# Kernel optimization log

Hardware: AMD Instinct MI355X
Metric: run time of the kernel (lower is better)

## Reference

```python
import jax, jax.numpy as jnp
import numpy as np

NL, H, PD, NH, NB = 4, 256, 64, 4, 65
B, L, AA = 2, 384, 48
DH = H // NH
MAX_REL = 32


def _ln(x, g, b):
    m = x.mean(-1, keepdims=True)
    v = ((x - m) ** 2).mean(-1, keepdims=True)
    return (x - m) * jax.lax.rsqrt(v + 1e-5) * g + b


def setup_inputs() -> dict:
    key = jax.random.key(0)
    ks = iter(jax.random.split(key, 64))
    w = lambda *s: jax.random.normal(next(ks), s, jnp.float32) * 0.02
    return dict(
        x=jax.random.normal(next(ks), (B, L, AA), jnp.float32),
        rp_w=w(AA, H), rp_b=jnp.zeros((H,), jnp.float32),
        pos_embed=w(L, H),
        pii_w=w(H, PD), pii_b=jnp.zeros((PD,), jnp.float32),
        pij_w=w(H, PD), pij_b=jnp.zeros((PD,), jnp.float32),
        rel_emb=w(2 * MAX_REL + 2, PD),
        ln_seq_g=jnp.ones((NL, H), jnp.float32), ln_seq_b=jnp.zeros((NL, H), jnp.float32),
        ln_pair_g=jnp.ones((NL, PD), jnp.float32), ln_pair_b=jnp.zeros((NL, PD), jnp.float32),
        pb_w=w(NL, PD, NH),
        in_w=w(NL, H, 3 * H), in_b=jnp.zeros((NL, 3 * H), jnp.float32),
        out_w=w(NL, H, H), out_b=jnp.zeros((NL, H), jnp.float32),
        ff_ln_g=jnp.ones((NL, H), jnp.float32), ff_ln_b=jnp.zeros((NL, H), jnp.float32),
        ff_w1=w(NL, H, 4 * H), ff_b1=jnp.zeros((NL, 4 * H), jnp.float32),
        ff_w2=w(NL, 4 * H, H), ff_b2=jnp.zeros((NL, H), jnp.float32),
        pu_ln_g=jnp.ones((NL, PD), jnp.float32), pu_ln_b=jnp.zeros((NL, PD), jnp.float32),
        pu_w1=w(NL, PD, PD), pu_b1=jnp.zeros((NL, PD), jnp.float32),
        pu_w2=w(NL, PD, PD), pu_b2=jnp.zeros((NL, PD), jnp.float32),
        outer_w=w(NL, 2 * H, PD), outer_b=jnp.zeros((NL, PD), jnp.float32),
        dh_ln_g=jnp.ones((PD,), jnp.float32), dh_ln_b=jnp.zeros((PD,), jnp.float32),
        dh_w1=w(PD, PD), dh_b1=jnp.zeros((PD,), jnp.float32),
        dh_w2=w(PD, NB), dh_b2=jnp.zeros((NB,), jnp.float32),
    )


def reference(x, rp_w, rp_b, pos_embed, pii_w, pii_b, pij_w, pij_b, rel_emb,
              ln_seq_g, ln_seq_b, ln_pair_g, ln_pair_b, pb_w, in_w, in_b,
              out_w, out_b, ff_ln_g, ff_ln_b, ff_w1, ff_b1, ff_w2, ff_b2,
              pu_ln_g, pu_ln_b, pu_w1, pu_b1, pu_w2, pu_b2, outer_w, outer_b,
              dh_ln_g, dh_ln_b, dh_w1, dh_b1, dh_w2, dh_b2):
    Bx, Lx, _ = x.shape
    gelu = lambda t: jax.nn.gelu(t, approximate=False)  # torch nn.GELU default (erf)
    h = x @ rp_w + rp_b + pos_embed[:Lx][None]
    # pair init: outer sum of two linear projections + clipped rel-pos embedding
    pair = (h @ pii_w + pii_b)[:, :, None, :] + (h @ pij_w + pij_b)[:, None, :, :]
    idx = jnp.arange(Lx)
    rel = jnp.clip(idx[None, :] - idx[:, None], -MAX_REL, MAX_REL) + MAX_REL  # (L,L)
    pair = pair + rel_emb[rel][None]
    for i in range(NL):
        seq_n = _ln(h, ln_seq_g[i], ln_seq_b[i])
        bias = _ln(pair, ln_pair_g[i], ln_pair_b[i]) @ pb_w[i]  # (B,L,L,NH)
        mask = bias.mean(axis=(0, 3))  # torch: permute->reshape(B*NH,L,L)->mean(0)
        qkv = seq_n @ in_w[i] + in_b[i]
        q, k, v = jnp.split(qkv, 3, axis=-1)
        q = q.reshape(Bx, Lx, NH, DH)
        k = k.reshape(Bx, Lx, NH, DH)
        v = v.reshape(Bx, Lx, NH, DH)
        scores = jnp.einsum('blhd,bmhd->bhlm', q, k) / float(np.sqrt(DH)) + mask
        attn = jax.nn.softmax(scores, axis=-1)
        o = jnp.einsum('bhlm,bmhd->blhd', attn, v).reshape(Bx, Lx, H)
        h = h + o @ out_w[i] + out_b[i]
        h = h + gelu(_ln(h, ff_ln_g[i], ff_ln_b[i]) @ ff_w1[i] + ff_b1[i]) @ ff_w2[i] + ff_b2[i]
        # outer_proj(cat([h_i, h_j])) == h@W[:H] outer-summed with h@W[H:]
        oi = h @ outer_w[i][:H]
        oj = h @ outer_w[i][H:]
        outer = oi[:, :, None, :] + oj[:, None, :, :] + outer_b[i]  # (B,L,L,PD)
        pair = pair + gelu(_ln(outer, pu_ln_g[i], pu_ln_b[i]) @ pu_w1[i] + pu_b1[i]) @ pu_w2[i] + pu_b2[i]
    logits = gelu(_ln(pair, dh_ln_g, dh_ln_b) @ dh_w1 + dh_b1) @ dh_w2 + dh_b2
    return (logits + jnp.swapaxes(logits, 1, 2)) / 2.0
```

## Files before the change

kernel.cpp:

```cpp
#include <hip/hip_runtime.h>
#include <math.h>

#define LSEQ 384
#define HD 256
#define PDIM 64
#define NHEAD 4
#define NBINS 65
#define BATCH 2
#define NTT (LSEQ / 16)
#define NTRI (NTT * (NTT + 1) / 2)

typedef __attribute__((ext_vector_type(8))) short bf16x8;
typedef __attribute__((ext_vector_type(16))) float f32x16;
typedef __attribute__((ext_vector_type(4))) float f32x4;
typedef __attribute__((ext_vector_type(4))) unsigned u32x4;
typedef __attribute__((ext_vector_type(4))) short s16x4;
#define MFMA32(a, b, c) __builtin_amdgcn_mfma_f32_32x32x16_bf16(a, b, c, 0, 0, 0)

template<int CTRL, int RMASK>
__device__ __forceinline__ float dpp_sum_step(float v) {
    int x = __builtin_amdgcn_update_dpp(0, __float_as_int(v), CTRL, RMASK, 0xf, true);
    return v + __int_as_float(x);
}
template<int CTRL, int RMASK>
__device__ __forceinline__ float dpp_max_step(float v) {
    int x = __builtin_amdgcn_update_dpp(__float_as_int(v), __float_as_int(v), CTRL, RMASK, 0xf, false);
    return fmaxf(v, __int_as_float(x));
}
__device__ __forceinline__ float wsum(float v) {
    v = dpp_sum_step<0x111, 0xf>(v);
    v = dpp_sum_step<0x112, 0xf>(v);
    v = dpp_sum_step<0x114, 0xf>(v);
    v = dpp_sum_step<0x118, 0xf>(v);
    v = dpp_sum_step<0x142, 0xa>(v);
    v = dpp_sum_step<0x143, 0xc>(v);
    return __int_as_float(__builtin_amdgcn_readlane(__float_as_int(v), 63));
}
__device__ __forceinline__ float wmax(float v) {
    v = dpp_max_step<0x111, 0xf>(v);
    v = dpp_max_step<0x112, 0xf>(v);
    v = dpp_max_step<0x114, 0xf>(v);
    v = dpp_max_step<0x118, 0xf>(v);
    v = dpp_max_step<0x142, 0xa>(v);
    v = dpp_max_step<0x143, 0xc>(v);
    return __int_as_float(__builtin_amdgcn_readlane(__float_as_int(v), 63));
}
__device__ __forceinline__ float gelu_erf(float x) {
    return 0.5f * x * (1.0f + erff(x * 0.70710678f));
}

__device__ __forceinline__ unsigned short f2bf(float x) {
    unsigned u = __float_as_uint(x);
    unsigned r = (u + 0x7fff + ((u >> 16) & 1)) >> 16;
    return (unsigned short)r;
}
__device__ __forceinline__ float bf2f(unsigned short h) {
    return __uint_as_float(((unsigned)h) << 16);
}
__device__ __forceinline__ void split_bf(float x, unsigned short& h, unsigned short& l) {
    h = f2bf(x);
    l = f2bf(x - bf2f(h));
}

__device__ __forceinline__ unsigned cvt_pk_bf(float lo, float hi) {
    unsigned r;
    asm("v_cvt_pk_bf16_f32 %0, %1, %2" : "=v"(r) : "v"(lo), "v"(hi));
    return r;
}
__device__ __forceinline__ void pack8(const float* v, u32x4& h, u32x4& l) {
#pragma unroll
    for (int j = 0; j < 4; ++j) {
        float a = v[2 * j], b = v[2 * j + 1];
        unsigned hp = cvt_pk_bf(a, b);
        float ra = a - __uint_as_float(hp << 16);
        float rb = b - __uint_as_float(hp & 0xffff0000u);
        h[j] = hp;
        l[j] = cvt_pk_bf(ra, rb);
    }
}
__device__ __forceinline__ bf16x8 as_bf(u32x4 x) {
    union { u32x4 u; bf16x8 b; } c; c.u = x; return c.b;
}
__device__ __forceinline__ bf16x8 ld8(const short* p) {
    s16x4 a = *(const s16x4*)p;
    s16x4 b = *(const s16x4*)(p + 4);
    bf16x8 r;
    r[0] = a[0]; r[1] = a[1]; r[2] = a[2]; r[3] = a[3];
    r[4] = b[0]; r[5] = b[1]; r[6] = b[2]; r[7] = b[3];
    return r;
}

__global__ void k_h_init(const float* __restrict__ x, const float* __restrict__ rp_w,
                         const float* __restrict__ rp_b, const float* __restrict__ pos,
                         float* __restrict__ h) {
    __shared__ float xs[48];
    int row = blockIdx.x;
    int l = row % LSEQ;
    int t = threadIdx.x;
    if (t < 48) xs[t] = x[row * 48 + t];
    __syncthreads();
    float acc = rp_b[t] + pos[l * HD + t];
#pragma unroll 8
    for (int a = 0; a < 48; ++a) acc += xs[a] * rp_w[a * HD + t];
    h[row * HD + t] = acc;
}

__global__ void k_proj2(const float* __restrict__ h, const float* __restrict__ wA,
                        const float* __restrict__ wB, const float* __restrict__ bA,
                        const float* __restrict__ bB, int center,
                        float* __restrict__ pA, float* __restrict__ pB) {
    __shared__ float hs[HD];
    int row = blockIdx.x;
    int t = threadIdx.x;
    hs[t] = h[row * HD + t];
    hs[t + 128] = h[row * HD + t + 128];
    __syncthreads();
    int col = t & 63;
    const float* w = (t < 64) ? wA : wB;
    const float* bias = (t < 64) ? bA : bB;
    float acc = bias ? bias[col] : 0.0f;
#pragma unroll 8
    for (int a = 0; a < HD; ++a) acc += hs[a] * w[a * PDIM + col];
    if (center) {
        float mean = wsum(acc) * (1.0f / PDIM);
        acc -= mean;
    }
    float* p = (t < 64) ? pA : pB;
    p[row * PDIM + col] = acc;
}

__global__ void __launch_bounds__(64) k_pair_init2(
    const float* __restrict__ pi, const float* __restrict__ pj,
    const float* __restrict__ rel_emb, const float* __restrict__ gpb,
    const float* __restrict__ cbv, float* __restrict__ pair,
    float* __restrict__ mask_out) {
    __shared__ __align__(16) float pt[32][65];
    int blk = blockIdx.x;
    int row = blk / 12, seg = blk % 12;
    int b = row / LSEQ, i = row % LSEQ;
    int t = threadIdx.x;
    int pl = t & 31, hq = t >> 5;
    int j0 = seg * 32;
    float piv = pi[row * 64 + t];
    const float* pjb = pj + ((size_t)b * LSEQ + j0) * 64;
#pragma unroll 8
    for (int j = 0; j < 32; ++j) {
        int r = j0 + j - i; r = r < -32 ? -32 : (r > 32 ? 32 : r); r += 32;
        pt[j][t] = piv + pjb[j * 64 + t] + rel_emb[r * 64 + t];
    }
    __syncthreads();
    float4* dst4 = (float4*)(pair + ((size_t)row * LSEQ + j0) * 64);
    for (int n = t; n < 512; n += 64) {
        int r2 = n >> 4, c4 = (n & 15) << 2;
        float4 g4 = { pt[r2][c4], pt[r2][c4 + 1], pt[r2][c4 + 2], pt[r2][c4 + 3] };
        dst4[n] = g4;
    }
    float vv[32];
    float sv = 0.0f;
#pragma unroll
    for (int c = 0; c < 32; ++c) { vv[c] = pt[pl][hq * 32 + c]; sv += vv[c]; }
    sv += __shfl_xor(sv, 32);
    float mean = sv * (1.0f / PDIM);
    float sd2 = 0.0f, sdg = 0.0f;
#pragma unroll
    for (int c = 0; c < 32; ++c) {
        float d = vv[c] - mean;
        sd2 = fmaf(d, d, sd2);
        sdg = fmaf(d, gpb[hq * 32 + c], sdg);
    }
    sd2 += __shfl_xor(sd2, 32);
    sdg += __shfl_xor(sdg, 32);
    float rsv = rsqrtf(sd2 * (1.0f / PDIM) + 1e-5f);
    float dot = rsv * sdg + cbv[0];
    if (hq == 0)
        atomicAdd(mask_out + i * LSEQ + j0 + pl, dot * (1.0f / (BATCH * NHEAD)));
}

__global__ void k_prep(const float* __restrict__ pu_ln_g, const float* __restrict__ pu_ln_b,
                       const float* __restrict__ pu_w1, const float* __restrict__ pu_b1,
                       const float* __restrict__ pu_w2,
                       const float* __restrict__ dh_ln_g, const float* __restrict__ dh_ln_b,
                       const float* __restrict__ dh_w1, const float* __restrict__ dh_b1,
                       const float* __restrict__ dh_w2,
                       unsigned short* __restrict__ w1hT, unsigned short* __restrict__ w1lT,
                       unsigned short* __restrict__ w2hT, unsigned short* __restrict__ w2lT,
                       float* __restrict__ b1p, float* __restrict__ w2c) {
    int i = blockIdx.x;
    int c = threadIdx.x;
    const float *g, *bb, *w1, *b1, *w2;
    int w2s;
    if (i < 4) { g = pu_ln_g + i * 64; bb = pu_ln_b + i * 64; w1 = pu_w1 + i * 4096;
                 b1 = pu_b1 + i * 64; w2 = pu_w2 + i * 4096; w2s = 64; }
    else       { g = dh_ln_g; bb = dh_ln_b; w1 = dh_w1; b1 = dh_b1; w2 = dh_w2; w2s = 65; }
    float accb = b1[c];
    for (int k = 0; k < 64; ++k) {
        float wv = w1[k * 64 + c];
        accb += bb[k] * wv;
        unsigned short h, l;
        split_bf(g[k] * wv, h, l);
        w1hT[i * 4096 + c * 64 + k] = h;
        w1lT[i * 4096 + c * 64 + k] = l;
        split_bf(w2[k * w2s + c], h, l);
        w2hT[i * 4096 + c * 64 + k] = h;
        w2lT[i * 4096 + c * 64 + k] = l;
    }
    b1p[i * 64 + c] = accb;
    if (i == 4) w2c[c] = dh_w2[c * 65 + 64];
}

__global__ void k_maskprep(const float* __restrict__ g, const float* __restrict__ bb,
                           const float* __restrict__ pbw, float* __restrict__ gp,
                           float* __restrict__ cb) {
    int li = blockIdx.x;
    int c = threadIdx.x;
    const float* pw = pbw + li * PDIM * NHEAD;
    float pbs = pw[c * 4] + pw[c * 4 + 1] + pw[c * 4 + 2] + pw[c * 4 + 3];
    gp[li * 64 + c] = g[li * 64 + c] * pbs;
    float s = wsum(bb[li * 64 + c] * pbs);
    if (c == 0) cb[li] = s;
}

__global__ void k_split_T(const float* __restrict__ src, unsigned short* __restrict__ dh,
                          unsigned short* __restrict__ dl, int K, int N,
                          int tiles_k, int tiles_n, size_t sstride, size_t dstride) {
    __shared__ float lds[64][65];
    int bid = blockIdx.x;
    int tpl = tiles_k * tiles_n;
    int layer = bid / tpl;
    int rest = bid % tpl;
    int kt = rest / tiles_n, nt = rest % tiles_n;
    const float* s = src + layer * sstride;
    int t = threadIdx.x, c = t & 63, r0 = t >> 6;
    for (int r = r0; r < 64; r += 4)
        lds[r][c] = s[(size_t)(kt * 64 + r) * N + nt * 64 + c];
    __syncthreads();
    unsigned short* oh = dh + layer * dstride;
    unsigned short* ol = dl + layer * dstride;
    for (int r = r0; r < 64; r += 4) {
        float v = lds[c][r];
        unsigned short h, l;
        split_bf(v, h, l);
        size_t o = (size_t)(nt * 64 + r) * K + kt * 64 + c;
        oh[o] = h;
        ol[o] = l;
    }
}

template<bool GELU>
__global__ void __launch_bounds__(64) k_gemm(
    const float* __restrict__ X, const unsigned short* __restrict__ wTh,
    const unsigned short* __restrict__ wTl, const float* __restrict__ bias,
    const float* __restrict__ R, float* __restrict__ OUT, int K, int N) {
    int idx = blockIdx.x;
    int lane = threadIdx.x & 63;
    int pl = lane & 31, hq = lane >> 5;
    int ntiles = N >> 5;
    int mt = idx / ntiles, nt = idx % ntiles;
    const float* xr = X + (size_t)(mt * 32 + pl) * K + 8 * hq;
    const unsigned short* bh = wTh + (size_t)(nt * 32 + pl) * K + 8 * hq;
    const unsigned short* bl = wTl + (size_t)(nt * 32 + pl) * K + 8 * hq;
    int n = nt * 32 + pl;
    float bv = bias[n];
    f32x16 acc;
#pragma unroll
    for (int r = 0; r < 16; ++r) {
        int mr = mt * 32 + (r & 3) + 8 * (r >> 2) + 4 * hq;
        acc[r] = bv + (R ? R[(size_t)mr * N + n] : 0.0f);
    }
#pragma unroll 4
    for (int s = 0; s < K; s += 16) {
        const f32x4* x4 = (const f32x4*)(xr + s);
        f32x4 xa = x4[0], xb = x4[1];
        float xv[8];
#pragma unroll
        for (int j = 0; j < 4; ++j) { xv[j] = xa[j]; xv[4 + j] = xb[j]; }
        u32x4 ah, al;
        pack8(xv, ah, al);
        bf16x8 bhv = *(const bf16x8*)(bh + s);
        bf16x8 blv = *(const bf16x8*)(bl + s);
        acc = MFMA32(as_bf(ah), bhv, acc);
        acc = MFMA32(as_bf(al), bhv, acc);
        acc = MFMA32(as_bf(ah), blv, acc);
    }
#pragma unroll
    for (int r = 0; r < 16; ++r) {
        int mr = mt * 32 + (r & 3) + 8 * (r >> 2) + 4 * hq;
        float v = acc[r];
        OUT[(size_t)mr * N + n] = GELU ? gelu_erf(v) : v;
    }
}

__global__ void k_ln_seq(const float* __restrict__ h, const float* __restrict__ g,
                         const float* __restrict__ b, float* __restrict__ out) {
    __shared__ float red[8];
    int row = blockIdx.x;
    int t = threadIdx.x;
    int w = t >> 6, lane = t & 63;
    float v = h[row * HD + t];
    float s = wsum(v);
    if (lane == 0) red[w] = s;
    __syncthreads();
    float mean = (red[0] + red[1] + red[2] + red[3]) * (1.0f / HD);
    float d = v - mean;
    float q = wsum(d * d);
    if (lane == 0) red[4 + w] = q;
    __syncthreads();
    float var = (red[4] + red[5] + red[6] + red[7]) * (1.0f / HD);
    out[row * HD + t] = d * rsqrtf(var + 1e-5f) * g[t] + b[t];
}

__global__ void k_attn(const float* __restrict__ qkv, const float* __restrict__ mask,
                       float* __restrict__ o) {
    __shared__ __align__(16) float qs[64];
    __shared__ float sc[LSEQ];
    __shared__ float red[8];
    __shared__ float op[4][64];
    int bid = blockIdx.x;
    int l = bid % LSEQ;
    int nh = (bid / LSEQ) & 3;
    int b = bid / (LSEQ * NHEAD);
    int t = threadIdx.x;
    int w = t >> 6, lane = t & 63;
    const float* qbase = qkv + ((size_t)(b * LSEQ + l)) * 768 + nh * 64;
    if (t < 64) qs[t] = qbase[t];
    __syncthreads();
    float lmax = -1e30f;
    float myv[2];
#pragma unroll
    for (int it = 0; it < 2; ++it) {
        int m = t + it * 256;
        if (m < LSEQ) {
            const float* kb = qkv + ((size_t)(b * LSEQ + m)) * 768 + 256 + nh * 64;
            const float4* k4 = (const float4*)kb;
            const float4* q4 = (const float4*)qs;
            float acc = 0.0f;
#pragma unroll
            for (int a = 0; a < 16; ++a) {
                float4 kv = k4[a], qv = q4[a];
                acc += qv.x * kv.x + qv.y * kv.y + qv.z * kv.z + qv.w * kv.w;
            }
            float s = acc * 0.125f + mask[l * LSEQ + m];
            myv[it] = s;
            lmax = fmaxf(lmax, s);
        } else myv[it] = -1e30f;
    }
    float wm = wmax(lmax);
    if (lane == 0) red[w] = wm;
    __syncthreads();
    float gmax = fmaxf(fmaxf(red[0], red[1]), fmaxf(red[2], red[3]));
    float lsum = 0.0f;
#pragma unroll
    for (int it = 0; it < 2; ++it) {
        int m = t + it * 256;
        if (m < LSEQ) {
            float e = expf(myv[it] - gmax);
            sc[m] = e;
            lsum += e;
        }
    }
    float ws = wsum(lsum);
    if (lane == 0) red[4 + w] = ws;
    __syncthreads();
    float inv = 1.0f / (red[4] + red[5] + red[6] + red[7]);
    int d = t & 63, gq = t >> 6;
    float part = 0.0f;
    for (int m = gq * 96; m < (gq + 1) * 96; ++m)
        part += sc[m] * qkv[((size_t)(b * LSEQ + m)) * 768 + 512 + nh * 64 + d];
    op[gq][d] = part;
    __syncthreads();
    if (t < 64) {
        float ov = (op[0][t] + op[1][t] + op[2][t] + op[3][t]) * inv;
        o[((size_t)(b * LSEQ + l)) * HD + nh * 64 + t] = ov;
    }
}

template<bool DIST>
__global__ void __launch_bounds__(256) k_pair_upd(
    const float* __restrict__ ojc,
    const float* __restrict__ oic,
    const unsigned short* __restrict__ w1hT, const unsigned short* __restrict__ w1lT,
    const float* __restrict__ b1p,
    const unsigned short* __restrict__ w2hT, const unsigned short* __restrict__ w2lT,
    const float* __restrict__ b2, float* __restrict__ pair,
    const float* __restrict__ gpb, const float* __restrict__ cbv,
    float* __restrict__ mask_out,
    const unsigned short* __restrict__ dw1h, const unsigned short* __restrict__ dw1l,
    const float* __restrict__ db1p,
    const unsigned short* __restrict__ dw2h, const unsigned short* __restrict__ dw2l,
    const float* __restrict__ w2c, const float* __restrict__ db2,
    float* __restrict__ outg) {
    __shared__ __align__(16) char smem[DIST ? 33344 : 17472];
    short (*lw)[64][68] = (short (*)[64][68])smem;
    int blk = blockIdx.x;
    int row = blk / 3, seg = blk % 3;
    int b = row / LSEQ;
    int t = threadIdx.x;
    int wave = t >> 6, lane = t & 63;
    int pl = lane & 31, hq = lane >> 5;
    int jj = wave * 32 + pl;
    int p = seg * 128 + jj;
    const float* ojr = ojc + ((size_t)b * LSEQ + p) * 64;
    const float* oir = oic + (size_t)row * 64;
    float* prp = pair + ((size_t)row * LSEQ + p) * 64;

#define STAGE2(srcA, srcB) \
    for (int idx = t; idx < 2048; idx += 256) { \
        int rr2 = idx >> 5, cc2 = (idx & 31) * 2; \
        *(unsigned*)&lw[0][rr2][cc2] = *(const unsigned*)(srcA + rr2 * 64 + cc2); \
        *(unsigned*)&lw[1][rr2][cc2] = *(const unsigned*)(srcB + rr2 * 64 + cc2); \
    }

    float v[32];
    {
        const f32x4* a4 = (const f32x4*)ojr;
        const f32x4* c4 = (const f32x4*)oir;
#pragma unroll
        for (int s = 0; s < 4; ++s) {
            f32x4 a = a4[4 * s + 2 * hq], aa = a4[4 * s + 2 * hq + 1];
            f32x4 c = c4[4 * s + 2 * hq], cc = c4[4 * s + 2 * hq + 1];
#pragma unroll
            for (int j = 0; j < 4; ++j) {
                v[8 * s + j] = a[j] + c[j];
                v[8 * s + 4 + j] = aa[j] + cc[j];
            }
        }
    }
    STAGE2(w1hT, w1lT)

    float ss = 0.0f;
#pragma unroll
    for (int i = 0; i < 32; ++i) ss = fmaf(v[i], v[i], ss);
    ss += __shfl_xor(ss, 32);
    float rs = rsqrtf(ss * (1.0f / PDIM) + 1e-5f);
#pragma unroll
    for (int i = 0; i < 32; ++i) v[i] *= rs;
    u32x4 zh[4], zl[4];
#pragma unroll
    for (int s = 0; s < 4; ++s) pack8(v + 8 * s, zh[s], zl[s]);

    const f32x4* b14 = (const f32x4*)b1p;
    f32x4 bi0[4], bi1[4];
#pragma unroll
    for (int g = 0; g < 4; ++g) { bi0[g] = b14[2 * g + hq]; bi1[g] = b14[8 + 2 * g + hq]; }

    __syncthreads();

    f32x16 acc0, acc1;
#pragma unroll
    for (int r = 0; r < 16; ++r) {
        acc0[r] = bi0[r >> 2][r & 3];
        acc1[r] = bi1[r >> 2][r & 3];
    }
#pragma unroll
    for (int s = 0; s < 4; ++s) {
        int ko = 16 * s + 8 * hq;
        bf16x8 a0h = ld8(&lw[0][pl][ko]);
        bf16x8 a0l = ld8(&lw[1][pl][ko]);
        bf16x8 a1h = ld8(&lw[0][32 + pl][ko]);
        bf16x8 a1l = ld8(&lw[1][32 + pl][ko]);
        bf16x8 zhs = as_bf(zh[s]), zls = as_bf(zl[s]);
        acc0 = MFMA32(a0h, zhs, acc0);
        acc0 = MFMA32(a0h, zls, acc0);
        acc0 = MFMA32(a0l, zhs, acc0);
        acc1 = MFMA32(a1h, zhs, acc1);
        acc1 = MFMA32(a1h, zls, acc1);
        acc1 = MFMA32(a1l, zhs, acc1);
    }
    __syncthreads();
    STAGE2(w2hT, w2lT)

    float u0[16], u1[16];
#pragma unroll
    for (int r = 0; r < 16; ++r) { u0[r] = gelu_erf(acc0[r]); u1[r] = gelu_erf(acc1[r]); }

    f32x4 r0[4], r1[4], q0[4], q1[4];
    {
        const f32x4* pr4 = (const f32x4*)prp;
        const f32x4* b24 = (const f32x4*)b2;
#pragma unroll
        for (int g = 0; g < 4; ++g) {
            r0[g] = pr4[2 * g + hq];
            r1[g] = pr4[8 + 2 * g + hq];
            q0[g] = b24[2 * g + hq];
            q1[g] = b24[8 + 2 * g + hq];
        }
    }

    float rA0[4], rB0[4], rA1[4], rB1[4];
#pragma unroll
    for (int i = 0; i < 4; ++i) {
        rA0[i] = __shfl_xor(hq ? u0[i] : u0[4 + i], 32);
        rB0[i] = __shfl_xor(hq ? u0[8 + i] : u0[12 + i], 32);
        rA1[i] = __shfl_xor(hq ? u1[i] : u1[4 + i], 32);
        rB1[i] = __shfl_xor(hq ? u1[8 + i] : u1[12 + i], 32);
    }
    u32x4 uh[4], ul[4];
#pragma unroll
    for (int s = 0; s < 4; ++s) {
        int tt = s >> 1, q = s & 1;
        float fg[8];
#pragma unroll
        for (int i = 0; i < 4; ++i) {
            float own_f = q ? (tt ? u1[8 + i] : u0[8 + i]) : (tt ? u1[i] : u0[i]);
            float own_s = q ? (tt ? u1[12 + i] : u0[12 + i]) : (tt ? u1[4 + i] : u0[4 + i]);
            float rcv   = q ? (tt ? rB1[i] : rB0[i]) : (tt ? rA1[i] : rA0[i]);
            fg[i]     = hq ? rcv : own_f;
            fg[4 + i] = hq ? own_s : rcv;
        }
        pack8(fg, uh[s], ul[s]);
    }

    __syncthreads();

    f32x16 c0, c1;
#pragma unroll
    for (int r = 0; r < 16; ++r) {
        int g = r >> 2, i = r & 3;
        c0[r] = q0[g][i] + r0[g][i];
        c1[r] = q1[g][i] + r1[g][i];
    }
#pragma unroll
    for (int s = 0; s < 4; ++s) {
        int ko = 16 * s + 8 * hq;
        bf16x8 a0h = ld8(&lw[0][pl][ko]);
        bf16x8 a0l = ld8(&lw[1][pl][ko]);
        bf16x8 a1h = ld8(&lw[0][32 + pl][ko]);
        bf16x8 a1l = ld8(&lw[1][32 + pl][ko]);
        bf16x8 uhs = as_bf(uh[s]), uls = as_bf(ul[s]);
        c0 = MFMA32(a0h, uhs, c0);
        c0 = MFMA32(a0h, uls, c0);
        c0 = MFMA32(a0l, uhs, c0);
        c1 = MFMA32(a1h, uhs, c1);
        c1 = MFMA32(a1h, uls, c1);
        c1 = MFMA32(a1l, uhs, c1);
    }

    if constexpr (!DIST) {
        const f32x4* gp4 = (const f32x4*)gpb;
        f32x4 gp0[4], gp1[4];
#pragma unroll
        for (int g = 0; g < 4; ++g) { gp0[g] = gp4[2 * g + hq]; gp1[g] = gp4[8 + 2 * g + hq]; }
        float sv = 0.0f;
#pragma unroll
        for (int r = 0; r < 16; ++r) sv += c0[r] + c1[r];
        sv += __shfl_xor(sv, 32);
        float mean = sv * (1.0f / PDIM);
        float sd2 = 0.0f, sdg = 0.0f;
#pragma unroll 4
        for (int r = 0; r < 16; ++r) {
            int g = r >> 2, i = r & 3;
            float d0 = c0[r] - mean, d1 = c1[r] - mean;
            sd2 = fmaf(d0, d0, sd2);
            sd2 = fmaf(d1, d1, sd2);
            sdg = fmaf(d0, gp0[g][i], sdg);
            sdg = fmaf(d1, gp1[g][i], sdg);
        }
        sd2 += __shfl_xor(sd2, 32);
        sdg += __shfl_xor(sdg, 32);
        float rsv = rsqrtf(sd2 * (1.0f / PDIM) + 1e-5f);
        float dot = rsv * sdg + cbv[0];
        if (hq == 0)
            atomicAdd(mask_out + (row % LSEQ) * LSEQ + p, dot * (1.0f / (BATCH * NHEAD)));
        f32x4* pw4 = (f32x4*)prp;
#pragma unroll
        for (int g = 0; g < 4; ++g) {
            f32x4 s0, s1;
#pragma unroll
            for (int i = 0; i < 4; ++i) { s0[i] = c0[4 * g + i]; s1[i] = c1[4 * g + i]; }
            pw4[2 * g + hq] = s0;
            pw4[8 + 2 * g + hq] = s1;
        }
    } else {
        float ra[4], rb[4], rc[4], rd[4];
#pragma unroll
        for (int i = 0; i < 4; ++i) {
            ra[i] = __shfl_xor(hq ? c0[i] : c0[4 + i], 32);
            rb[i] = __shfl_xor(hq ? c0[8 + i] : c0[12 + i], 32);
            rc[i] = __shfl_xor(hq ? c1[i] : c1[4 + i], 32);
            rd[i] = __shfl_xor(hq ? c1[8 + i] : c1[12 + i], 32);
        }
        float v2[32];
#pragma unroll
        for (int i = 0; i < 4; ++i) {
            v2[i]      = hq ? ra[i] : c0[i];
            v2[4 + i]  = hq ? c0[4 + i] : ra[i];
            v2[8 + i]  = hq ? rb[i] : c0[8 + i];
            v2[12 + i] = hq ? c0[12 + i] : rb[i];
            v2[16 + i] = hq ? rc[i] : c1[i];
            v2[20 + i] = hq ? c1[4 + i] : rc[i];
            v2[24 + i] = hq ? rd[i] : c1[8 + i];
            v2[28 + i] = hq ? c1[12 + i] : rd[i];
        }
        __syncthreads();
        STAGE2(dw1h, dw1l)

        float sm = 0.0f;
#pragma unroll
        for (int i = 0; i < 32; ++i) sm += v2[i];
        sm += __shfl_xor(sm, 32);
        float mean = sm * (1.0f / PDIM);
        float ss2 = 0.0f;
#pragma unroll
        for (int i = 0; i < 32; ++i) { v2[i] -= mean; ss2 = fmaf(v2[i], v2[i], ss2); }
        ss2 += __shfl_xor(ss2, 32);
        float rs2 = rsqrtf(ss2 * (1.0f / PDIM) + 1e-5f);
#pragma unroll
        for (int i = 0; i < 32; ++i) v2[i] *= rs2;
#pragma unroll
        for (int s = 0; s < 4; ++s) pack8(v2 + 8 * s, zh[s], zl[s]);

        const f32x4* d14 = (const f32x4*)db1p;
        const f32x4* d24 = (const f32x4*)db2;
        const f32x4* wc4 = (const f32x4*)w2c;
        f32x4 di0[4], di1[4], e0[4], e1[4], wc0[4], wc1[4];
#pragma unroll
        for (int g = 0; g < 4; ++g) {
            di0[g] = d14[2 * g + hq]; di1[g] = d14[8 + 2 * g + hq];
            e0[g] = d24[2 * g + hq];  e1[g] = d24[8 + 2 * g + hq];
            wc0[g] = wc4[2 * g + hq]; wc1[g] = wc4[8 + 2 * g + hq];
        }
        __syncthreads();

#pragma unroll
        for (int r = 0; r < 16; ++r) {
            acc0[r] = di0[r >> 2][r & 3];
            acc1[r] = di1[r >> 2][r & 3];
        }
#pragma unroll
        for (int s = 0; s < 4; ++s) {
            int ko = 16 * s + 8 * hq;
            bf16x8 a0h = ld8(&lw[0][pl][ko]);
            bf16x8 a0l = ld8(&lw[1][pl][ko]);
            bf16x8 a1h = ld8(&lw[0][32 + pl][ko]);
            bf16x8 a1l = ld8(&lw[1][32 + pl][ko]);
            bf16x8 zhs = as_bf(zh[s]), zls = as_bf(zl[s]);
            acc0 = MFMA32(a0h, zhs, acc0);
            acc0 = MFMA32(a0h, zls, acc0);
            acc0 = MFMA32(a0l, zhs, acc0);
            acc1 = MFMA32(a1h, zhs, acc1);
            acc1 = MFMA32(a1h, zls, acc1);
            acc1 = MFMA32(a1l, zhs, acc1);
        }
        __syncthreads();
        STAGE2(dw2h, dw2l)

        float p64 = 0.0f;
#pragma unroll
        for (int r = 0; r < 16; ++r) {
            int g = r >> 2, i = r & 3;
            u0[r] = gelu_erf(acc0[r]);
            u1[r] = gelu_erf(acc1[r]);
            p64 = fmaf(u0[r], wc0[g][i], p64);
            p64 = fmaf(u1[r], wc1[g][i], p64);
        }
        p64 += __shfl_xor(p64, 32);
#pragma unroll
        for (int i = 0; i < 4; ++i) {
            rA0[i] = __shfl_xor(hq ? u0[i] : u0[4 + i], 32);
            rB0[i] = __shfl_xor(hq ? u0[8 + i] : u0[12 + i], 32);
            rA1[i] = __shfl_xor(hq ? u1[i] : u1[4 + i], 32);
            rB1[i] = __shfl_xor(hq ? u1[8 + i] : u1[12 + i], 32);
        }
#pragma unroll
        for (int s = 0; s < 4; ++s) {
            int tt = s >> 1, q = s & 1;
            float fg[8];
#pragma unroll
            for (int i = 0; i < 4; ++i) {
                float own_f = q ? (tt ? u1[8 + i] : u0[8 + i]) : (tt ? u1[i] : u0[i]);
                float own_s = q ? (tt ? u1[12 + i] : u0[12 + i]) : (tt ? u1[4 + i] : u0[4 + i]);
                float rcv   = q ? (tt ? rB1[i] : rB0[i]) : (tt ? rA1[i] : rA0[i]);
                fg[i]     = hq ? rcv : own_f;
                fg[4 + i] = hq ? own_s : rcv;
            }
            pack8(fg, uh[s], ul[s]);
        }
        __syncthreads();

#pragma unroll
        for (int r = 0; r < 16; ++r) {
            c0[r] = e0[r >> 2][r & 3];
            c1[r] = e1[r >> 2][r & 3];
        }
#pragma unroll
        for (int s = 0; s < 4; ++s) {
            int ko = 16 * s + 8 * hq;
            bf16x8 a0h = ld8(&lw[0][pl][ko]);
            bf16x8 a0l = ld8(&lw[1][pl][ko]);
            bf16x8 a1h = ld8(&lw[0][32 + pl][ko]);
            bf16x8 a1l = ld8(&lw[1][32 + pl][ko]);
            bf16x8 uhs = as_bf(uh[s]), uls = as_bf(ul[s]);
            c0 = MFMA32(a0h, uhs, c0);
            c0 = MFMA32(a0h, uls, c0);
            c0 = MFMA32(a0l, uhs, c0);
            c1 = MFMA32(a1h, uhs, c1);
            c1 = MFMA32(a1h, uls, c1);
            c1 = MFMA32(a1l, uhs, c1);
        }
        __syncthreads();
        float (*pt)[65] = (float (*)[65])smem;
#pragma unroll
        for (int r = 0; r < 16; ++r) {
            int rr = (r & 3) + 8 * (r >> 2) + 4 * hq;
            pt[jj][rr] = c0[r];
            pt[jj][32 + rr] = c1[r];
        }
        if (hq == 0) pt[jj][64] = p64 + db2[64];
        __syncthreads();
        float4* dst = (float4*)(outg + ((size_t)row * LSEQ + seg * 128) * NBINS);
        const float4* srcl = (const float4*)&pt[0][0];
        for (int n = t; n < 128 * NBINS / 4; n += 256) dst[n] = srcl[n];
    }
#undef STAGE2
}

__global__ void k_sym(float* __restrict__ out) {
    int u = blockIdx.x;
    int b = 0;
    if (u >= NTRI) { b = 1; u -= NTRI; }
    int lt = 0, rem = NTT;
    while (u >= rem) { u -= rem; ++lt; --rem; }
    int mt = lt + u;
    int t = threadIdx.x;
    int g = t >> 6, lane = t & 63;
    float* ob = out + (size_t)b * LSEQ * LSEQ * NBINS;
    for (int e = g; e < 256; e += 4) {
        int i = e >> 4, j = e & 15;
        if (lt == mt && j < i) continue;
        size_t ia = ((size_t)(lt * 16 + i) * LSEQ + (mt * 16 + j)) * NBINS;
        size_t ib = ((size_t)(mt * 16 + j) * LSEQ + (lt * 16 + i)) * NBINS;
        for (int k = lane; k < NBINS; k += 64) {
            float a = ob[ia + k], c = ob[ib + k];
            float vv = 0.5f * (a + c);
            ob[ia + k] = vv;
            if (ia != ib) ob[ib + k] = vv;
        }
    }
}

extern "C" void kernel_launch(void* const* d_in, const int* in_sizes, int n_in,
                              void* d_out, int out_size, void* d_ws, size_t ws_size,
                              hipStream_t stream) {
    const float* x        = (const float*)d_in[0];
    const float* rp_w     = (const float*)d_in[1];
    const float* rp_b     = (const float*)d_in[2];
    const float* pos      = (const float*)d_in[3];
    const float* pii_w    = (const float*)d_in[4];
    const float* pii_b    = (const float*)d_in[5];
    const float* pij_w    = (const float*)d_in[6];
    const float* pij_b    = (const float*)d_in[7];
    const float* rel_emb  = (const float*)d_in[8];
    const float* ln_seq_g = (const float*)d_in[9];
    const float* ln_seq_b = (const float*)d_in[10];
    const float* ln_pair_g= (const float*)d_in[11];
    const float* ln_pair_b= (const float*)d_in[12];
    const float* pb_w     = (const float*)d_in[13];
    const float* in_w     = (const float*)d_in[14];
    const float* in_b     = (const float*)d_in[15];
    const float* out_w    = (const float*)d_in[16];
    const float* out_b    = (const float*)d_in[17];
    const float* ff_ln_g  = (const float*)d_in[18];
    const float* ff_ln_b  = (const float*)d_in[19];
    const float* ff_w1    = (const float*)d_in[20];
    const float* ff_b1    = (const float*)d_in[21];
    const float* ff_w2    = (const float*)d_in[22];
    const float* ff_b2    = (const float*)d_in[23];
    const float* pu_ln_g  = (const float*)d_in[24];
    const float* pu_ln_b  = (const float*)d_in[25];
    const float* pu_w1    = (const float*)d_in[26];
    const float* pu_b1    = (const float*)d_in[27];
    const float* pu_w2    = (const float*)d_in[28];
    const float* pu_b2    = (const float*)d_in[29];
    const float* outer_w  = (const float*)d_in[30];
    const float* outer_b  = (const float*)d_in[31];
    const float* dh_ln_g  = (const float*)d_in[32];
    const float* dh_ln_b  = (const float*)d_in[33];
    const float* dh_w1    = (const float*)d_in[34];
    const float* dh_b1    = (const float*)d_in[35];
    const float* dh_w2    = (const float*)d_in[36];
    const float* dh_b2    = (const float*)d_in[37];
    float* outp = (float*)d_out;

    float* W = (float*)d_ws;
    float* h    = W;  W += BATCH * LSEQ * HD;
    float* sn   = W;  W += BATCH * LSEQ * HD;
    float* qkv  = W;  W += BATCH * LSEQ * 3 * HD;
    float* ob   = W;  W += BATCH * LSEQ * HD;
    float* mid  = W;  W += BATCH * LSEQ * 4 * HD;
    float* maskA= W;  W += LSEQ * LSEQ;
    float* maskB= W;  W += LSEQ * LSEQ;
    float* poi  = W;  W += BATCH * LSEQ * PDIM;
    float* poj  = W;  W += BATCH * LSEQ * PDIM;
    float* b1p  = W;  W += 5 * 64;
    float* w2c  = W;  W += 64;
    float* gpb  = W;  W += 4 * 64;
    float* cbv  = W;  W += 64;
    unsigned short* w1hT = (unsigned short*)W;  W += 5 * 2048;
    unsigned short* w1lT = (unsigned short*)W;  W += 5 * 2048;
    unsigned short* w2hT = (unsigned short*)W;  W += 5 * 2048;
    unsigned short* w2lT = (unsigned short*)W;  W += 5 * 2048;
    unsigned short* qwT_h = (unsigned short*)W;  W += 4 * 196608 / 2;
    unsigned short* qwT_l = (unsigned short*)W;  W += 4 * 196608 / 2;
    unsigned short* owT_h = (unsigned short*)W;  W += 4 * 65536 / 2;
    unsigned short* owT_l = (unsigned short*)W;  W += 4 * 65536 / 2;
    unsigned short* f1T_h = (unsigned short*)W;  W += 4 * 262144 / 2;
    unsigned short* f1T_l = (unsigned short*)W;  W += 4 * 262144 / 2;
    unsigned short* f2T_h = (unsigned short*)W;  W += 4 * 262144 / 2;
    unsigned short* f2T_l = (unsigned short*)W;  W += 4 * 262144 / 2;
    float* pair = W;  W += (size_t)BATCH * LSEQ * LSEQ * PDIM;

    const int rows = BATCH * LSEQ;

    k_prep<<<5, 64, 0, stream>>>(pu_ln_g, pu_ln_b, pu_w1, pu_b1, pu_w2,
                                 dh_ln_g, dh_ln_b, dh_w1, dh_b1, dh_w2,
                                 w1hT, w1lT, w2hT, w2lT, b1p, w2c);
    k_maskprep<<<4, 64, 0, stream>>>(ln_pair_g, ln_pair_b, pb_w, gpb, cbv);
    k_split_T<<<4 * 4 * 12, 256, 0, stream>>>(in_w,  qwT_h, qwT_l, 256, 768,  4, 12, 196608, 196608);
    k_split_T<<<4 * 4 * 4,  256, 0, stream>>>(out_w, owT_h, owT_l, 256, 256,  4, 4,  65536,  65536);
    k_split_T<<<4 * 4 * 16, 256, 0, stream>>>(ff_w1, f1T_h, f1T_l, 256, 1024, 4, 16, 262144, 262144);
    k_split_T<<<4 * 16 * 4, 256, 0, stream>>>(ff_w2, f2T_h, f2T_l, 1024, 256, 16, 4, 262144, 262144);
    k_h_init<<<rows, 256, 0, stream>>>(x, rp_w, rp_b, pos, h);
    k_proj2<<<rows, 128, 0, stream>>>(h, pii_w, pij_w, pii_b, pij_b, 0, poi, poj);
    hipMemsetAsync(maskA, 0, LSEQ * LSEQ * sizeof(float), stream);
    k_pair_init2<<<rows * 12, 64, 0, stream>>>(poi, poj, rel_emb, gpb, cbv, pair, maskA);

    float* mcur = maskA;
    float* mnext = maskB;
    for (int i = 0; i < 4; ++i) {
        k_ln_seq<<<rows, 256, 0, stream>>>(h, ln_seq_g + i * HD, ln_seq_b + i * HD, sn);
        k_gemm<false><<<576, 64, 0, stream>>>(sn, qwT_h + i * 196608, qwT_l + i * 196608,
                                              in_b + i * 768, nullptr, qkv, 256, 768);
        k_attn<<<BATCH * NHEAD * LSEQ, 256, 0, stream>>>(qkv, mcur, ob);
        k_gemm<false><<<192, 64, 0, stream>>>(ob, owT_h + i * 65536, owT_l + i * 65536,
                                              out_b + i * 256, h, h, 256, 256);
        k_ln_seq<<<rows, 256, 0, stream>>>(h, ff_ln_g + i * HD, ff_ln_b + i * HD, sn);
        k_gemm<true><<<768, 64, 0, stream>>>(sn, f1T_h + i * 262144, f1T_l + i * 262144,
                                             ff_b1 + i * 1024, nullptr, mid, 256, 1024);
        k_gemm<false><<<192, 64, 0, stream>>>(mid, f2T_h + i * 262144, f2T_l + i * 262144,
                                              ff_b2 + i * 256, h, h, 1024, 256);
        k_proj2<<<rows, 128, 0, stream>>>(h, outer_w + i * 2 * HD * PDIM,
                                          outer_w + i * 2 * HD * PDIM + HD * PDIM,
                                          outer_b + i * PDIM, nullptr, 1, poi, poj);
        if (i < 3) {
            hipMemsetAsync(mnext, 0, LSEQ * LSEQ * sizeof(float), stream);
            k_pair_upd<false><<<rows * 3, 256, 0, stream>>>(
                poj, poi,
                w1hT + i * 4096, w1lT + i * 4096, b1p + i * 64,
                w2hT + i * 4096, w2lT + i * 4096, pu_b2 + i * PDIM, pair,
                gpb + (i + 1) * 64, cbv + (i + 1), mnext,
                nullptr, nullptr, nullptr, nullptr, nullptr, nullptr, nullptr, nullptr);
            float* tmp = mcur; mcur = mnext; mnext = tmp;
        } else {
            k_pair_upd<true><<<rows * 3, 256, 0, stream>>>(
                poj, poi,
                w1hT + 3 * 4096, w1lT + 3 * 4096, b1p + 3 * 64,
                w2hT + 3 * 4096, w2lT + 3 * 4096, pu_b2 + 3 * PDIM, pair,
                nullptr, nullptr, nullptr,
                w1hT + 4 * 4096, w1lT + 4 * 4096, b1p + 4 * 64,
                w2hT + 4 * 4096, w2lT + 4 * 4096, w2c, dh_b2, outp);
        }
    }

    k_sym<<<2 * NTRI, 256, 0, stream>>>(outp);
}
```

Before: 1.050 ms.

## Fuse sequence LayerNorm into GEMM prologue and use fast erf for GELU

Removes the separate k_ln_seq kernels before the QKV and FF1 GEMMs. The LayerNorm gain is folded into the pre-split weights, and its bias is folded into a precomputed GEMM bias. Each GEMM wave now computes row mean and variance itself before normalising its input on the fly. GELU now uses an Abramowitz-Stegun erf polynomial with hardware rcp/exp instead of erff, which trades some accuracy and recomputes row statistics redundantly in every N-tile block.

```diff
diff --git a/kernel.cpp b/kernel.cpp
--- a/kernel.cpp
+++ b/kernel.cpp
@@ -45,8 +45,23 @@
     v = dpp_max_step<0x143, 0xc>(v);
     return __int_as_float(__builtin_amdgcn_readlane(__float_as_int(v), 63));
 }
+
+__device__ __forceinline__ float fast_rcp(float x) {
+    float r; asm("v_rcp_f32 %0, %1" : "=v"(r) : "v"(x)); return r;
+}
+__device__ __forceinline__ float fast_exp2(float x) {
+    float r; asm("v_exp_f32 %0, %1" : "=v"(r) : "v"(x)); return r;
+}
 __device__ __forceinline__ float gelu_erf(float x) {
-    return 0.5f * x * (1.0f + erff(x * 0.70710678f));
+    float z = x * 0.70710678f;
+    float az = fabsf(z);
+    float t = fast_rcp(fmaf(0.3275911f, az, 1.0f));
+    float p = fmaf(fmaf(fmaf(fmaf(1.061405429f, t, -1.453152027f), t,
+                  1.421413741f), t, -0.284496736f), t, 0.254829592f) * t;
+    float e = fast_exp2(az * az * -1.44269504f);
+    float er = fmaf(-p, e, 1.0f);
+    er = x < 0.0f ? -er : er;
+    return 0.5f * x * (1.0f + er);
 }
 
 __device__ __forceinline__ unsigned short f2bf(float x) {
@@ -220,7 +235,8 @@
     if (c == 0) cb[li] = s;
 }
 
-__global__ void k_split_T(const float* __restrict__ src, unsigned short* __restrict__ dh,
+__global__ void k_split_T(const float* __restrict__ src, const float* __restrict__ g,
+                          unsigned short* __restrict__ dh,
                           unsigned short* __restrict__ dl, int K, int N,
                           int tiles_k, int tiles_n, size_t sstride, size_t dstride) {
     __shared__ float lds[64][65];
@@ -236,8 +252,9 @@
     __syncthreads();
     unsigned short* oh = dh + layer * dstride;
     unsigned short* ol = dl + layer * dstride;
+    float gs = g ? g[layer * K + kt * 64 + c] : 1.0f;
     for (int r = r0; r < 64; r += 4) {
-        float v = lds[c][r];
+        float v = lds[c][r] * gs;
         unsigned short h, l;
         split_bf(v, h, l);
         size_t o = (size_t)(nt * 64 + r) * K + kt * 64 + c;
@@ -246,7 +263,21 @@
     }
 }
 
-template<bool GELU>
+__global__ void k_biasfold(const float* __restrict__ bin, const float* __restrict__ lnb,
+                           const float* __restrict__ w, int K, int N, size_t wstride,
+                           float* __restrict__ bout) {
+    int blk = blockIdx.x;
+    int npb = N >> 6;
+    int layer = blk / npb;
+    int n = (blk % npb) * 64 + threadIdx.x;
+    const float* wl = w + layer * wstride;
+    const float* lb = lnb + layer * K;
+    float acc = bin[layer * N + n];
+    for (int k = 0; k < K; ++k) acc = fmaf(lb[k], wl[(size_t)k * N + n], acc);
+    bout[layer * N + n] = acc;
+}
+
+template<bool GELU, bool LN>
 __global__ void __launch_bounds__(64) k_gemm(
     const float* __restrict__ X, const unsigned short* __restrict__ wTh,
     const unsigned short* __restrict__ wTl, const float* __restrict__ bias,
@@ -261,6 +292,25 @@
     const unsigned short* bl = wTl + (size_t)(nt * 32 + pl) * K + 8 * hq;
     int n = nt * 32 + pl;
     float bv = bias[n];
+    float mean = 0.0f, rsv = 1.0f;
+    if constexpr (LN) {
+        float sm = 0.0f, sq = 0.0f;
+        for (int s = 0; s < K; s += 16) {
+            const f32x4* x4 = (const f32x4*)(xr + s);
+            f32x4 xa = x4[0], xb = x4[1];
+#pragma unroll
+            for (int j = 0; j < 4; ++j) {
+                sm += xa[j] + xb[j];
+                sq = fmaf(xa[j], xa[j], sq);
+                sq = fmaf(xb[j], xb[j], sq);
+            }
+        }
+        sm += __shfl_xor(sm, 32);
+        sq += __shfl_xor(sq, 32);
+        float kinv = 1.0f / (float)K;
+        mean = sm * kinv;
+        rsv = rsqrtf(sq * kinv - mean * mean + 1e-5f);
+    }
     f32x16 acc;
 #pragma unroll
     for (int r = 0; r < 16; ++r) {
@@ -273,7 +323,14 @@
         f32x4 xa = x4[0], xb = x4[1];
         float xv[8];
 #pragma unroll
-        for (int j = 0; j < 4; ++j) { xv[j] = xa[j]; xv[4 + j] = xb[j]; }
+        for (int j = 0; j < 4; ++j) {
+            if constexpr (LN) {
+                xv[j]     = (xa[j] - mean) * rsv;
+                xv[4 + j] = (xb[j] - mean) * rsv;
+            } else {
+                xv[j] = xa[j]; xv[4 + j] = xb[j];
+            }
+        }
         u32x4 ah, al;
         pack8(xv, ah, al);
         bf16x8 bhv = *(const bf16x8*)(bh + s);
@@ -288,25 +345,6 @@
         float v = acc[r];
         OUT[(size_t)mr * N + n] = GELU ? gelu_erf(v) : v;
     }
-}
-
-__global__ void k_ln_seq(const float* __restrict__ h, const float* __restrict__ g,
-                         const float* __restrict__ b, float* __restrict__ out) {
-    __shared__ float red[8];
-    int row = blockIdx.x;
-    int t = threadIdx.x;
-    int w = t >> 6, lane = t & 63;
-    float v = h[row * HD + t];
-    float s = wsum(v);
-    if (lane == 0) red[w] = s;
-    __syncthreads();
-    float mean = (red[0] + red[1] + red[2] + red[3]) * (1.0f / HD);
-    float d = v - mean;
-    float q = wsum(d * d);
-    if (lane == 0) red[4 + w] = q;
-    __syncthreads();
-    float var = (red[4] + red[5] + red[6] + red[7]) * (1.0f / HD);
-    out[row * HD + t] = d * rsqrtf(var + 1e-5f) * g[t] + b[t];
 }
 
 __global__ void k_attn(const float* __restrict__ qkv, const float* __restrict__ mask,
@@ -783,7 +821,6 @@
 
     float* W = (float*)d_ws;
     float* h    = W;  W += BATCH * LSEQ * HD;
-    float* sn   = W;  W += BATCH * LSEQ * HD;
     float* qkv  = W;  W += BATCH * LSEQ * 3 * HD;
     float* ob   = W;  W += BATCH * LSEQ * HD;
     float* mid  = W;  W += BATCH * LSEQ * 4 * HD;
@@ -795,6 +832,8 @@
     float* w2c  = W;  W += 64;
     float* gpb  = W;  W += 4 * 64;
     float* cbv  = W;  W += 64;
+    float* qb_f = W;  W += 4 * 768;
+    float* fb_f = W;  W += 4 * 1024;
     unsigned short* w1hT = (unsigned short*)W;  W += 5 * 2048;
     unsigned short* w1lT = (unsigned short*)W;  W += 5 * 2048;
     unsigned short* w2hT = (unsigned short*)W;  W += 5 * 2048;
@@ -815,10 +854,12 @@
                                  dh_ln_g, dh_ln_b, dh_w1, dh_b1, dh_w2,
                                  w1hT, w1lT, w2hT, w2lT, b1p, w2c);
     k_maskprep<<<4, 64, 0, stream>>>(ln_pair_g, ln_pair_b, pb_w, gpb, cbv);
-    k_split_T<<<4 * 4 * 12, 256, 0, stream>>>(in_w,  qwT_h, qwT_l, 256, 768,  4, 12, 196608, 196608);
-    k_split_T<<<4 * 4 * 4,  256, 0, stream>>>(out_w, owT_h, owT_l, 256, 256,  4, 4,  65536,  65536);
-    k_split_T<<<4 * 4 * 16, 256, 0, stream>>>(ff_w1, f1T_h, f1T_l, 256, 1024, 4, 16, 262144, 262144);
-    k_split_T<<<4 * 16 * 4, 256, 0, stream>>>(ff_w2, f2T_h, f2T_l, 1024, 256, 16, 4, 262144, 262144);
+    k_split_T<<<4 * 4 * 12, 256, 0, stream>>>(in_w,  ln_seq_g, qwT_h, qwT_l, 256, 768,  4, 12, 196608, 196608);
+    k_split_T<<<4 * 4 * 4,  256, 0, stream>>>(out_w, nullptr,  owT_h, owT_l, 256, 256,  4, 4,  65536,  65536);
+    k_split_T<<<4 * 4 * 16, 256, 0, stream>>>(ff_w1, ff_ln_g,  f1T_h, f1T_l, 256, 1024, 4, 16, 262144, 262144);
+    k_split_T<<<4 * 16 * 4, 256, 0, stream>>>(ff_w2, nullptr,  f2T_h, f2T_l, 1024, 256, 16, 4, 262144, 262144);
+    k_biasfold<<<4 * 12, 64, 0, stream>>>(in_b,  ln_seq_b, in_w,  256, 768,  196608, qb_f);
+    k_biasfold<<<4 * 16, 64, 0, stream>>>(ff_b1, ff_ln_b,  ff_w1, 256, 1024, 262144, fb_f);
     k_h_init<<<rows, 256, 0, stream>>>(x, rp_w, rp_b, pos, h);
     k_proj2<<<rows, 128, 0, stream>>>(h, pii_w, pij_w, pii_b, pij_b, 0, poi, poj);
     hipMemsetAsync(maskA, 0, LSEQ * LSEQ * sizeof(float), stream);
@@ -827,17 +868,15 @@
     float* mcur = maskA;
     float* mnext = maskB;
     for (int i = 0; i < 4; ++i) {
-        k_ln_seq<<<rows, 256, 0, stream>>>(h, ln_seq_g + i * HD, ln_seq_b + i * HD, sn);
-        k_gemm<false><<<576, 64, 0, stream>>>(sn, qwT_h + i * 196608, qwT_l + i * 196608,
-                                              in_b + i * 768, nullptr, qkv, 256, 768);
+        k_gemm<false, true><<<576, 64, 0, stream>>>(h, qwT_h + i * 196608, qwT_l + i * 196608,
+                                                    qb_f + i * 768, nullptr, qkv, 256, 768);
         k_attn<<<BATCH * NHEAD * LSEQ, 256, 0, stream>>>(qkv, mcur, ob);
-        k_gemm<false><<<192, 64, 0, stream>>>(ob, owT_h + i * 65536, owT_l + i * 65536,
-                                              out_b + i * 256, h, h, 256, 256);
-        k_ln_seq<<<rows, 256, 0, stream>>>(h, ff_ln_g + i * HD, ff_ln_b + i * HD, sn);
-        k_gemm<true><<<768, 64, 0, stream>>>(sn, f1T_h + i * 262144, f1T_l + i * 262144,
-                                             ff_b1 + i * 1024, nullptr, mid, 256, 1024);
-        k_gemm<false><<<192, 64, 0, stream>>>(mid, f2T_h + i * 262144, f2T_l + i * 262144,
-                                              ff_b2 + i * 256, h, h, 1024, 256);
+        k_gemm<false, false><<<192, 64, 0, stream>>>(ob, owT_h + i * 65536, owT_l + i * 65536,
+                                                     out_b + i * 256, h, h, 256, 256);
+        k_gemm<true, true><<<768, 64, 0, stream>>>(h, f1T_h + i * 262144, f1T_l + i * 262144,
+                                                   fb_f + i * 1024, nullptr, mid, 256, 1024);
+        k_gemm<false, false><<<192, 64, 0, stream>>>(mid, f2T_h + i * 262144, f2T_l + i * 262144,
+                                                     ff_b2 + i * 256, h, h, 1024, 256);
         k_proj2<<<rows, 128, 0, stream>>>(h, outer_w + i * 2 * HD * PDIM,
                                           outer_w + i * 2 * HD * PDIM + HD * PDIM,
                                           outer_b + i * PDIM, nullptr, 1, poi, poj);
```

After: 1.142 ms. 8.7% more time.
